# Performance work log

Measured on AMD Instinct MI355X. Metric: run time of the kernel, lower is better.

The kernel has to match this reference:

```python
import jax, jax.numpy as jnp
import numpy as np

B, T, D, H, DH, M, L, OUT = 512, 49, 256, 8, 32, 1024, 4, 151
DI = H * DH
THR = 0.02


def _ln(x, g, b):
    mu = x.mean(-1, keepdims=True)
    v = ((x - mu) ** 2).mean(-1, keepdims=True)
    return (x - mu) / jnp.sqrt(v + 1e-5) * g + b


def setup_inputs() -> dict:
    key = jax.random.key(0)
    ks = iter(jax.random.split(key, 64))

    def W(*s):
        return jax.random.normal(next(ks), s, jnp.float32) * 0.02

    inp = {}
    for n in ['img0', 'img1', 'p0', 'p1', 'p2']:
        inp[n] = jax.random.normal(next(ks), (B, T, D), jnp.float32)
    inp['idx'] = jax.random.randint(next(ks), (3, 2, B, T), 0, T, dtype=jnp.int32)
    # two transformer encoders (image/point), stacked over [encoder=2, layer=L]
    inp['enc_ln1g'] = jnp.ones((2, L, D)); inp['enc_ln1b'] = jnp.zeros((2, L, D))
    inp['enc_wqkv'] = W(2, L, D, 3 * DI)
    inp['enc_wo'] = W(2, L, DI, D); inp['enc_bo'] = jnp.zeros((2, L, D))
    inp['enc_ln2g'] = jnp.ones((2, L, D)); inp['enc_ln2b'] = jnp.zeros((2, L, D))
    inp['enc_w1'] = W(2, L, D, M); inp['enc_b1'] = jnp.zeros((2, L, M))
    inp['enc_w2'] = W(2, L, M, D); inp['enc_b2'] = jnp.zeros((2, L, D))
    # per-depth score nets (PredictorLG)
    inp['sc_lng'] = jnp.ones((L, D)); inp['sc_lnb'] = jnp.zeros((L, D))
    inp['sc_w1'] = W(L, D, D); inp['sc_b1'] = jnp.zeros((L, D))
    inp['sc_w2'] = W(L, D, D // 2); inp['sc_b2'] = jnp.zeros((L, D // 2))
    inp['sc_w3'] = W(L, D // 2, 2); inp['sc_b3'] = jnp.zeros((L, 2))
    # per-depth patch MLPs (FFN dim->mlp_dim->mlp_dim->dim, 3 layers)
    inp['pm_w1'] = W(L, D, M); inp['pm_b1'] = jnp.zeros((L, M))
    inp['pm_w2'] = W(L, M, M); inp['pm_b2'] = jnp.zeros((L, M))
    inp['pm_w3'] = W(L, M, D); inp['pm_b3'] = jnp.zeros((L, D))
    # mlp head
    inp['hd_lng'] = jnp.ones((D,)); inp['hd_lnb'] = jnp.zeros((D,))
    inp['hd_w1'] = W(D, M); inp['hd_b1'] = jnp.zeros((M,))
    inp['hd_w2'] = W(M, OUT); inp['hd_b2'] = jnp.zeros((OUT,))
    return inp


def reference(img0, img1, p0, p1, p2, idx,
              enc_ln1g, enc_ln1b, enc_wqkv, enc_wo, enc_bo,
              enc_ln2g, enc_ln2b, enc_w1, enc_b1, enc_w2, enc_b2,
              sc_lng, sc_lnb, sc_w1, sc_b1, sc_w2, sc_b2, sc_w3, sc_b3,
              pm_w1, pm_b1, pm_w2, pm_b2, pm_w3, pm_b3,
              hd_lng, hd_lnb, hd_w1, hd_b1, hd_w2, hd_b2):

    def layer(x, e, i):
        # pre-norm attention
        h = _ln(x, enc_ln1g[e, i], enc_ln1b[e, i])
        qkv = h @ enc_wqkv[e, i]                      # [B,T,3*DI]
        q, k, v = jnp.split(qkv, 3, axis=-1)
        q = q.reshape(B, T, H, DH); k = k.reshape(B, T, H, DH); v = v.reshape(B, T, H, DH)
        a = jax.nn.softmax(jnp.einsum('bqhd,bkhd->bhqk', q, k) * (DH ** -0.5), -1)
        o = jnp.einsum('bhqk,bkhd->bqhd', a, v).reshape(B, T, DI)
        x = x + o @ enc_wo[e, i] + enc_bo[e, i]
        # pre-norm FFN
        h = _ln(x, enc_ln2g[e, i], enc_ln2b[e, i])
        return x + jax.nn.gelu(h @ enc_w1[e, i] + enc_b1[e, i]) @ enc_w2[e, i] + enc_b2[e, i]

    image_feats = [img0, img1]
    point_feats = [p0, p1, p2]
    pred_scores = []
    for i in range(L):
        image_tokens = [layer(f, 0, i) for f in image_feats]
        point_tokens = [layer(f, 1, i) for f in point_feats]
        allt = jnp.concatenate(image_tokens + point_tokens, axis=1)  # [B, 5*T, D]
        h = _ln(allt, sc_lng[i], sc_lnb[i])
        h = jax.nn.gelu(h @ sc_w1[i] + sc_b1[i])
        h = jax.nn.gelu(h @ sc_w2[i] + sc_b2[i])
        scores = jax.nn.softmax(h @ sc_w3[i] + sc_b3[i], -1)[:, :, 0]  # [B, 5*T]
        pred_scores.append(scores)
        mask = (scores > THR).astype(jnp.int32)[..., None]            # [B,5*T,1]
        fm = mask.astype(allt.dtype)
        fnm = (-mask - 1).astype(allt.dtype)  # torch ~int_mask is bitwise NOT: ~1=-2, ~0=-1 (faithful)
        image_feats = [image_tokens[j] * fm[:, j * T:(j + 1) * T]
                       + image_tokens[1 - j] * fnm[:, j * T:(j + 1) * T] for j in range(2)]

        def patch_mlp(x):
            h2 = jax.nn.gelu(x @ pm_w1[i] + pm_b1[i])
            h2 = jax.nn.gelu(h2 @ pm_w2[i] + pm_b2[i])
            return h2 @ pm_w3[i] + pm_b3[i]

        new_p = []
        for k2 in range(3):
            s0 = 2 * T + k2 * T
            g0 = jnp.take_along_axis(image_tokens[0], idx[k2, 0][..., None], axis=1)
            g1 = jnp.take_along_axis(image_tokens[1], idx[k2, 1][..., None], axis=1)
            patch = patch_mlp(g0) + patch_mlp(g1)
            new_p.append(point_tokens[k2] * fm[:, s0:s0 + T] + patch * fnm[:, s0:s0 + T])
        point_feats = new_p

    pooled = jnp.concatenate(image_feats + point_feats, axis=1).max(axis=1)  # [B, D]
    h = _ln(pooled, hd_lng, hd_lnb)
    smplx = jax.nn.gelu(h @ hd_w1 + hd_b1) @ hd_w2 + hd_b2                   # [B, OUT]
    pred_score = jnp.concatenate(pred_scores, axis=1)                         # [B, L*5*T]
    return smplx, pred_score
```

## Files before the change

kernel.cpp:

```cpp
#include <hip/hip_runtime.h>
#include <math.h>

#define B_ 512
#define T_ 49
#define D_ 256
#define M_ 1024
#define L_ 4
#define OUT_ 151
#define BT_ 25088
#define NTOK5 (5*BT_)
#define THRESH 0.02f

typedef __bf16 bf16x8 __attribute__((ext_vector_type(8)));
typedef float f32x4 __attribute__((ext_vector_type(4)));
typedef unsigned short us;

__device__ __forceinline__ float gelu_t(float x){
    float u = 0.7978845608028654f * x * (1.0f + 0.044715f*x*x);
    float e = __expf(-2.0f*u);
    return __fdividef(x, 1.0f + e);
}
__device__ __forceinline__ us f2bf(float f){
    unsigned int u = __float_as_uint(f);
    u += 0x7fffu + ((u>>16)&1u);
    return (us)(u>>16);
}
__device__ __forceinline__ float bf2f(us h){
    return __uint_as_float(((unsigned int)h)<<16);
}
__device__ __forceinline__ void gload16(const void* g, void* l){
    __builtin_amdgcn_global_load_lds(
        (const __attribute__((address_space(1))) void*)g,
        (__attribute__((address_space(3))) void*)l, 16, 0, 0);
}

__global__ void copy_in_kernel(const float* __restrict__ a0, const float* __restrict__ a1,
                               const float* __restrict__ a2, const float* __restrict__ a3,
                               const float* __restrict__ a4, float* __restrict__ dst){
    size_t i = (size_t)blockIdx.x*256 + threadIdx.x;
    if (i >= (size_t)NTOK5*64) return;
    int slot = (int)(i / ((size_t)BT_*64));
    size_t off = i % ((size_t)BT_*64);
    const float* src = slot==0?a0: slot==1?a1: slot==2?a2: slot==3?a3: a4;
    ((float4*)dst)[i] = ((const float4*)src)[off];
}

__global__ void xcvt_kernel(const float* __restrict__ x, us* __restrict__ y, int nrows){
    size_t i = (size_t)blockIdx.x*256 + threadIdx.x;
    if (i >= (size_t)nrows*64) return;
    float4 v = ((const float4*)x)[i];
    ushort4 o; o.x=f2bf(v.x); o.y=f2bf(v.y); o.z=f2bf(v.z); o.w=f2bf(v.w);
    ((ushort4*)y)[i] = o;
}

template<bool OBF>
__global__ void ln_kernel(const float* __restrict__ x, const float* __restrict__ g,
                          const float* __restrict__ b, void* __restrict__ y, int nrows){
    int row = blockIdx.x*4 + (threadIdx.x>>6);
    if (row >= nrows) return;
    int lane = threadIdx.x & 63;
    float4 v = ((const float4*)(x + (size_t)row*D_))[lane];
    float s  = v.x+v.y+v.z+v.w;
    float sq = v.x*v.x + v.y*v.y + v.z*v.z + v.w*v.w;
    #pragma unroll
    for (int o=32;o;o>>=1){ s += __shfl_xor(s,o,64); sq += __shfl_xor(sq,o,64); }
    float mu = s*(1.0f/256.0f);
    float rstd = rsqrtf(sq*(1.0f/256.0f) - mu*mu + 1e-5f);
    float4 gv = ((const float4*)g)[lane];
    float4 bv = ((const float4*)b)[lane];
    float o0 = (v.x-mu)*rstd*gv.x + bv.x;
    float o1 = (v.y-mu)*rstd*gv.y + bv.y;
    float o2 = (v.z-mu)*rstd*gv.z + bv.z;
    float o3 = (v.w-mu)*rstd*gv.w + bv.w;
    if (OBF){
        ushort4 o4; o4.x=f2bf(o0); o4.y=f2bf(o1); o4.z=f2bf(o2); o4.w=f2bf(o3);
        ((ushort4*)((us*)y + (size_t)row*D_))[lane] = o4;
    } else {
        float4 o4; o4.x=o0; o4.y=o1; o4.z=o2; o4.w=o3;
        ((float4*)((float*)y + (size_t)row*D_))[lane] = o4;
    }
}

__global__ void wtrans_kernel(const float* __restrict__ W, us* __restrict__ Wt,
                              int K, int N){
    int g = blockIdx.z;
    __shared__ float t[32][33];
    int k0 = blockIdx.y*32, n0 = blockIdx.x*32;
    int tx = threadIdx.x&31, ty = threadIdx.x>>5;
    for (int r=ty; r<32; r+=8){
        int k = k0+r, n = n0+tx;
        t[r][tx] = (k<K && n<N) ? W[(size_t)g*K*N + (size_t)k*N + n] : 0.f;
    }
    __syncthreads();
    for (int r=ty; r<32; r+=8){
        int n = n0+r, k = k0+tx;
        if (n<N && k<K) Wt[(size_t)g*N*K + (size_t)n*K + k] = f2bf(t[tx][r]);
    }
}

__global__ void wtrans_pad_kernel(const float* __restrict__ W, us* __restrict__ Wt,
                                  int K, int Nsrc, int Ndst){
    __shared__ float t[32][33];
    int k0 = blockIdx.y*32, n0 = blockIdx.x*32;
    int tx = threadIdx.x&31, ty = threadIdx.x>>5;
    for (int r=ty; r<32; r+=8){
        int k = k0+r, n = n0+tx;
        t[r][tx] = (k<K && n<Nsrc) ? W[(size_t)k*Nsrc + n] : 0.f;
    }
    __syncthreads();
    for (int r=ty; r<32; r+=8){
        int n = n0+r, k = k0+tx;
        if (n<Ndst && k<K) Wt[(size_t)n*K + k] = f2bf(t[tx][r]);
    }
}

__global__ void padb_kernel(const float* __restrict__ b, float* __restrict__ o,
                            int Nsrc, int Ndst){
    int i = blockIdx.x*256 + threadIdx.x;
    if (i < Ndst) o[i] = (i < Nsrc) ? b[i] : 0.f;
}

__global__ void headcopy_kernel(const float* __restrict__ src, float* __restrict__ dst){
    int i = blockIdx.x*256 + threadIdx.x;
    if (i >= B_*OUT_) return;
    int r = i / OUT_, c = i % OUT_;
    dst[i] = src[(size_t)r*256 + c];
}

__device__ __forceinline__ void gemm_compute(const us* As, const us* Bs,
        int wr, int wc, int lr, int kg, f32x4 (&acc)[4][4]){
    bf16x8 av[4], bv[4];
    #pragma unroll
    for (int mi=0;mi<4;mi++){
        int r = wr*64 + mi*16 + lr;
        av[mi] = *(const bf16x8*)(&As[r*32 + ((kg ^ ((r>>1)&3))<<3)]);
    }
    #pragma unroll
    for (int ni=0;ni<4;ni++){
        int c = wc*64 + ni*16 + lr;
        bv[ni] = *(const bf16x8*)(&Bs[c*32 + ((kg ^ ((c>>1)&3))<<3)]);
    }
    #pragma unroll
    for (int mi=0;mi<4;mi++)
        #pragma unroll
        for (int ni=0;ni<4;ni++)
            acc[mi][ni] = __builtin_amdgcn_mfma_f32_16x16x32_bf16(av[mi], bv[ni], acc[mi][ni], 0, 0, 0);
}

template<int ACT, int RIN, bool OBF>
__global__ __launch_bounds__(256) void mfma_gemm(
    const us* __restrict__ A, const us* __restrict__ Wt,
    const float* __restrict__ bias, const void* __restrict__ resid,
    void* __restrict__ Cout, int Mr, int N, int K)
{
    __shared__ __align__(16) us SM[3*8192];
    const int nwg  = gridDim.x*gridDim.y;
    const int flat = blockIdx.y*gridDim.x + blockIdx.x;
    const int qq = nwg>>3, rr = nwg&7;
    const int xcd = flat&7, sidx = flat>>3;
    const int logical = (xcd<rr) ? (xcd*(qq+1)+sidx) : (rr*(qq+1)+(xcd-rr)*qq+sidx);
    const int bn = (logical % gridDim.x)*128;
    const int bm = (logical / gridDim.x)*128;
    const int tid = threadIdx.x;
    const int lane = tid&63, w = tid>>6;
    const int wr = w>>1, wc = w&1;
    const int lr = lane&15, kg = lane>>4;
    f32x4 acc[4][4] = {};

    const int j0 = tid, j1 = tid+256;
    const int row0 = j0>>2, row1 = j1>>2;
    const int k8s0 = (j0&3) ^ ((row0>>1)&3);
    const int k8s1 = (j1&3) ^ ((row1>>1)&3);
    int ga0 = bm+row0; if (ga0>=Mr) ga0=Mr-1;
    int ga1 = bm+row1; if (ga1>=Mr) ga1=Mr-1;
    int gb0 = bn+row0; if (gb0>=N) gb0=N-1;
    int gb1 = bn+row1; if (gb1>=N) gb1=N-1;
    const us* a0p = A  + (size_t)ga0*K + k8s0*8;
    const us* a1p = A  + (size_t)ga1*K + k8s1*8;
    const us* b0p = Wt + (size_t)gb0*K + k8s0*8;
    const us* b1p = Wt + (size_t)gb1*K + k8s1*8;

    const int nk = K >> 5;
    #define STAGEK(t_) { us* nb_ = SM + ((t_)%3)*8192; int k0_ = (t_)<<5; \
        gload16(a0p + k0_, nb_ + j0*8); \
        gload16(a1p + k0_, nb_ + j1*8); \
        gload16(b0p + k0_, nb_ + 4096 + j0*8); \
        gload16(b1p + k0_, nb_ + 4096 + j1*8); }
    STAGEK(0); STAGEK(1);
    for (int t=0; t<nk; ++t){
        if (t+1 < nk) asm volatile("s_waitcnt vmcnt(4)" ::: "memory");
        else          asm volatile("s_waitcnt vmcnt(0)" ::: "memory");
        __builtin_amdgcn_s_barrier();
        __builtin_amdgcn_sched_barrier(0);
        if (t+2 < nk) STAGEK(t+2);
        const us* cb = SM + (t%3)*8192;
        gemm_compute(cb, cb+4096, wr, wc, lr, kg, acc);
    }
    #undef STAGEK
    __syncthreads();

    if (OBF && RIN==0){
        us* Cs16 = (us*)SM;
        #pragma unroll
        for (int mi=0;mi<4;mi++){
            #pragma unroll
            for (int ni=0;ni<4;ni++){
                #pragma unroll
                for (int r4=0;r4<4;r4++){
                    int row = wr*64 + mi*16 + kg*4 + r4;
                    int col = wc*64 + ni*16 + lr;
                    float v = acc[mi][ni][r4];
                    if (bias) v += bias[bn + col];
                    if (ACT==1) v = gelu_t(v);
                    int h = ((row>>2)&3) | ((row&1)<<2);
                    int punit = (col>>3) ^ h;
                    Cs16[row*128 + punit*8 + (col&7)] = f2bf(v);
                }
            }
        }
        __syncthreads();
        {
            int rbase = tid>>3, seg = tid&7;
            #pragma unroll
            for (int pass=0; pass<8; ++pass){
                int row = rbase + (pass>>1)*32;
                int half = pass&1;
                int grow = bm + row;
                if (grow < Mr){
                    int h = ((row>>2)&3) | ((row&1)<<2);
                    int punit = (half*8+seg) ^ h;
                    *(uint4*)((us*)Cout + (size_t)grow*N + bn + half*64 + seg*8)
                        = *(const uint4*)&Cs16[row*128 + punit*8];
                }
            }
        }
        return;
    }

    float* Cs = (float*)SM;
    #pragma unroll
    for (int er=0; er<2; er++){
        #pragma unroll
        for (int ml=0; ml<2; ml++){
            int mi = er*2 + ml;
            #pragma unroll
            for (int ni=0;ni<4;ni++){
                #pragma unroll
                for (int r4=0;r4<4;r4++){
                    int lrow = wr*32 + ml*16 + kg*4 + r4;
                    int lcol = wc*64 + ni*16 + lr;
                    int pcol = lcol ^ (((lrow>>2)&1)<<4);
                    float v = acc[mi][ni][r4];
                    if (bias) v += bias[bn + lcol];
                    if (ACT==1) v = gelu_t(v);
                    Cs[lrow*128 + pcol] = v;
                }
            }
        }
        __syncthreads();
        #pragma unroll
        for (int s=0; s<2; s++){
            int lrow = (tid>>3) + s*32;
            int tseg = tid&7;
            int pseg = tseg ^ ((lrow>>2)&1);
            const float4* src = (const float4*)&Cs[lrow*128 + pseg*16];
            float4 v0=src[0], v1=src[1], v2=src[2], v3=src[3];
            int grow = bm + (lrow>>5)*64 + (er*2 + ((lrow>>4)&1))*16 + (lrow&15);
            int gcol = bn + tseg*16;
            if (grow < Mr){
                if (RIN==1){
                    const float4* rp = (const float4*)((const float*)resid + (size_t)grow*N + gcol);
                    float4 r0=rp[0], r1=rp[1], r2=rp[2], r3=rp[3];
                    v0.x+=r0.x; v0.y+=r0.y; v0.z+=r0.z; v0.w+=r0.w;
                    v1.x+=r1.x; v1.y+=r1.y; v1.z+=r1.z; v1.w+=r1.w;
                    v2.x+=r2.x; v2.y+=r2.y; v2.z+=r2.z; v2.w+=r2.w;
                    v3.x+=r3.x; v3.y+=r3.y; v3.z+=r3.z; v3.w+=r3.w;
                } else if (RIN==2){
                    const uint4* rp = (const uint4*)((const us*)resid + (size_t)grow*N + gcol);
                    uint4 u0=rp[0], u1=rp[1];
                    v0.x+=bf2f((us)(u0.x&0xffff)); v0.y+=bf2f((us)(u0.x>>16));
                    v0.z+=bf2f((us)(u0.y&0xffff)); v0.w+=bf2f((us)(u0.y>>16));
                    v1.x+=bf2f((us)(u0.z&0xffff)); v1.y+=bf2f((us)(u0.z>>16));
                    v1.z+=bf2f((us)(u0.w&0xffff)); v1.w+=bf2f((us)(u0.w>>16));
                    v2.x+=bf2f((us)(u1.x&0xffff)); v2.y+=bf2f((us)(u1.x>>16));
                    v2.z+=bf2f((us)(u1.y&0xffff)); v2.w+=bf2f((us)(u1.y>>16));
                    v3.x+=bf2f((us)(u1.z&0xffff)); v3.y+=bf2f((us)(u1.z>>16));
                    v3.z+=bf2f((us)(u1.w&0xffff)); v3.w+=bf2f((us)(u1.w>>16));
                }
                if (OBF){
                    unsigned int w0 = (unsigned)f2bf(v0.x) | ((unsigned)f2bf(v0.y)<<16);
                    unsigned int w1 = (unsigned)f2bf(v0.z) | ((unsigned)f2bf(v0.w)<<16);
                    unsigned int w2 = (unsigned)f2bf(v1.x) | ((unsigned)f2bf(v1.y)<<16);
                    unsigned int w3 = (unsigned)f2bf(v1.z) | ((unsigned)f2bf(v1.w)<<16);
                    unsigned int w4 = (unsigned)f2bf(v2.x) | ((unsigned)f2bf(v2.y)<<16);
                    unsigned int w5 = (unsigned)f2bf(v2.z) | ((unsigned)f2bf(v2.w)<<16);
                    unsigned int w6 = (unsigned)f2bf(v3.x) | ((unsigned)f2bf(v3.y)<<16);
                    unsigned int w7 = (unsigned)f2bf(v3.z) | ((unsigned)f2bf(v3.w)<<16);
                    uint4* op = (uint4*)((us*)Cout + (size_t)grow*N + gcol);
                    uint4 u0; u0.x=w0; u0.y=w1; u0.z=w2; u0.w=w3;
                    uint4 u1; u1.x=w4; u1.y=w5; u1.z=w6; u1.w=w7;
                    op[0]=u0; op[1]=u1;
                } else {
                    float4* op = (float4*)((float*)Cout + (size_t)grow*N + gcol);
                    op[0]=v0; op[1]=v1; op[2]=v2; op[3]=v3;
                }
            }
        }
        __syncthreads();
    }
}

__global__ __launch_bounds__(128) void attn_kernel(const us* __restrict__ qkv,
                                                   us* __restrict__ o){
    __shared__ float ks[2][T_][36], vs[2][T_][36];
    const int w = threadIdx.x >> 6, lane = threadIdx.x & 63;
    const int bh = blockIdx.x*2 + w;
    const int bb = bh >> 3, h = bh & 7;
    const us* base = qkv + (size_t)bb*T_*768 + h*32;
    if (lane < T_){
        const uint4* kp = (const uint4*)(base + (size_t)lane*768 + 256);
        const uint4* vp = (const uint4*)(base + (size_t)lane*768 + 512);
        #pragma unroll
        for (int j=0;j<4;j++){
            uint4 ku = kp[j], vu = vp[j];
            unsigned ka[4]={ku.x,ku.y,ku.z,ku.w}, va[4]={vu.x,vu.y,vu.z,vu.w};
            #pragma unroll
            for (int e=0;e<4;e++){
                ks[w][lane][j*8+e*2]   = bf2f((us)(ka[e]&0xffffu));
                ks[w][lane][j*8+e*2+1] = bf2f((us)(ka[e]>>16));
                vs[w][lane][j*8+e*2]   = bf2f((us)(va[e]&0xffffu));
                vs[w][lane][j*8+e*2+1] = bf2f((us)(va[e]>>16));
            }
        }
    }
    __syncthreads();
    if (lane >= T_) return;
    float q[32];
    {
        const uint4* qp = (const uint4*)(base + (size_t)lane*768);
        #pragma unroll
        for (int j=0;j<4;j++){
            uint4 qu = qp[j];
            unsigned qa[4]={qu.x,qu.y,qu.z,qu.w};
            #pragma unroll
            for (int e=0;e<4;e++){
                q[j*8+e*2]   = bf2f((us)(qa[e]&0xffffu));
                q[j*8+e*2+1] = bf2f((us)(qa[e]>>16));
            }
        }
    }
    float S[T_];
    #pragma unroll
    for (int c=0;c<T_;c++){
        float acc = 0.f;
        #pragma unroll
        for (int d=0;d<32;d++) acc += q[d]*ks[w][c][d];
        S[c] = acc*0.17677669529663687f;
    }
    float m = S[0];
    #pragma unroll
    for (int c=1;c<T_;c++) m = fmaxf(m, S[c]);
    float sum = 0.f;
    #pragma unroll
    for (int c=0;c<T_;c++){ S[c] = __expf(S[c]-m); sum += S[c]; }
    float inv = __fdividef(1.f, sum);
    float oa[32];
    #pragma unroll
    for (int d=0;d<32;d++) oa[d] = 0.f;
    #pragma unroll
    for (int c=0;c<T_;c++){
        float p2 = S[c]*inv;
        #pragma unroll
        for (int d=0;d<32;d++) oa[d] += p2*vs[w][c][d];
    }
    unsigned* op = (unsigned*)(o + ((size_t)bb*T_ + lane)*256 + h*32);
    #pragma unroll
    for (int j=0;j<16;j++)
        op[j] = (unsigned)f2bf(oa[2*j]) | ((unsigned)f2bf(oa[2*j+1])<<16);
}

__global__ void score_kernel(const us* __restrict__ s2, const float* __restrict__ w3,
                             const float* __restrict__ b3, float* __restrict__ sc,
                             float* __restrict__ pred, int layer, int row0, int nrows){
    int lr = blockIdx.x*256 + threadIdx.x;
    if (lr >= nrows) return;
    int row = row0 + lr;
    int s = row / BT_;
    int r = row % BT_;
    int b = r / T_;
    int t = r % T_;
    const uint4* xv = (const uint4*)(s2 + (size_t)lr*128);
    float l0 = b3[0], l1 = b3[1];
    #pragma unroll
    for (int q=0;q<16;q++){
        uint4 u = xv[q];
        unsigned int uu[4] = {u.x,u.y,u.z,u.w};
        #pragma unroll
        for (int e=0;e<4;e++){
            float fa = bf2f((us)(uu[e]&0xffff));
            float fb = bf2f((us)(uu[e]>>16));
            int d = q*8 + e*2;
            l0 += fa*w3[d*2]     + fb*w3[(d+1)*2];
            l1 += fa*w3[d*2+1]   + fb*w3[(d+1)*2+1];
        }
    }
    float m = fmaxf(l0,l1);
    float e0 = __expf(l0-m), e1 = __expf(l1-m);
    float sc0 = __fdividef(e0, e0+e1);
    sc[b*(5*T_) + s*T_ + t] = sc0;
    pred[(size_t)b*(L_*5*T_) + (size_t)layer*(5*T_) + s*T_ + t] = sc0;
}

__global__ void img_fuse_kernel(float* __restrict__ X, const float* __restrict__ sc){
    size_t i = (size_t)blockIdx.x*256 + threadIdx.x;
    if (i >= (size_t)BT_*64) return;
    int row = (int)(i>>6), d4 = (int)(i&63);
    int b = row / T_, t = row % T_;
    float s0 = sc[b*(5*T_) + t];
    float s1 = sc[b*(5*T_) + T_ + t];
    float fm0  = (s0 > THRESH)? 1.f : 0.f;
    float fnm0 = -fm0 - 1.f;
    float fm1  = (s1 > THRESH)? 1.f : 0.f;
    float fnm1 = -fm1 - 1.f;
    float4* p0 = ((float4*)(X + (size_t)row*D_)) + d4;
    float4* p1 = ((float4*)(X + ((size_t)BT_ + row)*D_)) + d4;
    float4 a0 = *p0, a1 = *p1;
    float4 r0, r1;
    r0.x = a0.x*fm0 + a1.x*fnm0;  r0.y = a0.y*fm0 + a1.y*fnm0;
    r0.z = a0.z*fm0 + a1.z*fnm0;  r0.w = a0.w*fm0 + a1.w*fnm0;
    r1.x = a1.x*fm1 + a0.x*fnm1;  r1.y = a1.y*fm1 + a0.y*fnm1;
    r1.z = a1.z*fm1 + a0.z*fnm1;  r1.w = a1.w*fm1 + a0.w*fnm1;
    *p0 = r0; *p1 = r1;
}

__global__ void pt_fuse_gather_kernel(float* __restrict__ X, const us* __restrict__ PM,
                                      const int* __restrict__ idx, const float* __restrict__ sc){
    size_t i = (size_t)blockIdx.x*256 + threadIdx.x;
    if (i >= (size_t)3*BT_*64) return;
    int vrow = (int)(i>>6), d4 = (int)(i&63);
    int k2 = vrow / BT_, grow = vrow % BT_;
    int b = grow / T_, t = grow % T_;
    float s = sc[b*(5*T_) + (2+k2)*T_ + t];
    float fm  = (s > THRESH)? 1.f : 0.f;
    float fnm = -fm - 1.f;
    int i0 = idx[(size_t)(k2*2+0)*BT_ + grow];
    int i1 = idx[(size_t)(k2*2+1)*BT_ + grow];
    uint2 u0 = ((const uint2*)(PM + ((size_t)b*T_ + i0)*D_))[d4];
    uint2 u1 = ((const uint2*)(PM + ((size_t)BT_ + (size_t)b*T_ + i1)*D_))[d4];
    float p0 = bf2f((us)(u0.x&0xffff)) + bf2f((us)(u1.x&0xffff));
    float p1 = bf2f((us)(u0.x>>16))    + bf2f((us)(u1.x>>16));
    float p2 = bf2f((us)(u0.y&0xffff)) + bf2f((us)(u1.y&0xffff));
    float p3 = bf2f((us)(u0.y>>16))    + bf2f((us)(u1.y>>16));
    float4* xp = ((float4*)(X + ((size_t)(2+k2)*BT_ + grow)*D_)) + d4;
    float4 a = *xp;
    float4 rr;
    rr.x = a.x*fm + p0*fnm;
    rr.y = a.y*fm + p1*fnm;
    rr.z = a.z*fm + p2*fnm;
    rr.w = a.w*fm + p3*fnm;
    *xp = rr;
}

__global__ void pool_kernel(const float* __restrict__ x, float* __restrict__ p){
    int i = blockIdx.x*256 + threadIdx.x;
    if (i >= B_*64) return;
    int b = i>>6, d4 = i&63;
    float4 m; m.x=m.y=m.z=m.w=-3.4e38f;
    for (int s=0;s<5;s++){
        const float4* bp = ((const float4*)(x + ((size_t)s*BT_ + (size_t)b*T_)*D_)) + d4;
        for (int t=0;t<T_;t++){
            float4 v = bp[(size_t)t*64];
            m.x=fmaxf(m.x,v.x); m.y=fmaxf(m.y,v.y); m.z=fmaxf(m.z,v.z); m.w=fmaxf(m.w,v.w);
        }
    }
    ((float4*)p)[i] = m;
}

static inline int cdiv(int a, int b){ return (a+b-1)/b; }

extern "C" void kernel_launch(void* const* d_in, const int* in_sizes, int n_in,
                              void* d_out, int out_size, void* d_ws, size_t ws_size,
                              hipStream_t stream)
{
    const float* in_img0 = (const float*)d_in[0];
    const float* in_img1 = (const float*)d_in[1];
    const float* in_p0   = (const float*)d_in[2];
    const float* in_p1   = (const float*)d_in[3];
    const float* in_p2   = (const float*)d_in[4];
    const int*   in_idx  = (const int*)d_in[5];
    const float* enc_ln1g = (const float*)d_in[6];
    const float* enc_ln1b = (const float*)d_in[7];
    const float* enc_wqkv = (const float*)d_in[8];
    const float* enc_wo   = (const float*)d_in[9];
    const float* enc_bo   = (const float*)d_in[10];
    const float* enc_ln2g = (const float*)d_in[11];
    const float* enc_ln2b = (const float*)d_in[12];
    const float* enc_w1   = (const float*)d_in[13];
    const float* enc_b1   = (const float*)d_in[14];
    const float* enc_w2   = (const float*)d_in[15];
    const float* enc_b2   = (const float*)d_in[16];
    const float* sc_lng   = (const float*)d_in[17];
    const float* sc_lnb   = (const float*)d_in[18];
    const float* sc_w1    = (const float*)d_in[19];
    const float* sc_b1    = (const float*)d_in[20];
    const float* sc_w2    = (const float*)d_in[21];
    const float* sc_b2    = (const float*)d_in[22];
    const float* sc_w3    = (const float*)d_in[23];
    const float* sc_b3    = (const float*)d_in[24];
    const float* pm_w1    = (const float*)d_in[25];
    const float* pm_b1    = (const float*)d_in[26];
    const float* pm_w2    = (const float*)d_in[27];
    const float* pm_b2    = (const float*)d_in[28];
    const float* pm_w3    = (const float*)d_in[29];
    const float* pm_b3    = (const float*)d_in[30];
    const float* hd_lng   = (const float*)d_in[31];
    const float* hd_lnb   = (const float*)d_in[32];
    const float* hd_w1    = (const float*)d_in[33];
    const float* hd_b1    = (const float*)d_in[34];
    const float* hd_w2    = (const float*)d_in[35];
    const float* hd_b2    = (const float*)d_in[36];

    char* p = (char*)d_ws;
    float* X   = (float*)p;  p += (size_t)5*BT_*D_*4;
    float* SCb = (float*)p;  p += (size_t)B_*5*T_*4;
    us* PM   = (us*)p; p += (size_t)2*BT_*D_*2;
    us* WQKV = (us*)p; p += (size_t)8*768*256*2;
    us* WWO  = (us*)p; p += (size_t)8*256*256*2;
    us* WW1  = (us*)p; p += (size_t)8*1024*256*2;
    us* WW2  = (us*)p; p += (size_t)8*256*1024*2;
    us* WS1  = (us*)p; p += (size_t)4*256*256*2;
    us* WS2  = (us*)p; p += (size_t)4*128*256*2;
    us* WP1  = (us*)p; p += (size_t)4*1024*256*2;
    us* WP2  = (us*)p; p += (size_t)4*1024*1024*2;
    us* WP3  = (us*)p; p += (size_t)4*256*1024*2;
    us* WH1  = (us*)p; p += (size_t)1024*256*2;
    us* WH2  = (us*)p; p += (size_t)256*1024*2;
    float* B2P  = (float*)p; p += (size_t)256*4;
    float* POOL = (float*)p; p += (size_t)B_*256*4;
    us*    HLNb = (us*)p;  p += (size_t)B_*256*2;
    us*    HMIDb= (us*)p;  p += (size_t)B_*1024*2;
    float* HOUT = (float*)p; p += (size_t)B_*256*4;
    size_t fixed = (size_t)(p - (char*)d_ws);
    long long poolb = (long long)ws_size - (long long)fixed;
    if (poolb < 0) poolb = 0;
    auto chunkOf = [&](long long perRow, int maxRows)->int{
        long long c = poolb / perRow;
        c = (c / T_) * T_;
        if (c < T_) c = T_;
        if (c > maxRows) c = maxRows;
        return (int)c;
    };
    auto evenC = [&](int total, int Cmax)->int{
        int nch = (total + Cmax - 1)/Cmax;
        int per = (total + nch - 1)/nch;
        per = ((per + T_ - 1)/T_)*T_;
        if (per > Cmax) per = Cmax;
        return per;
    };
    int CencMax = chunkOf(2560, 3*BT_);
    int CscMax  = chunkOf(1024, NTOK5);
    int CpmMax  = chunkOf(4096, 2*BT_);
    char* pb = p;
    us* eR1 = (us*)pb;
    us* eR2 = (us*)(pb + (size_t)CencMax*512);
    us* eR3 = eR1;
    us* sR1 = (us*)pb;
    us* sS1 = (us*)(pb + (size_t)CscMax*512);
    us* sS2 = sR1;
    us* m1  = (us*)pb;
    us* m2  = (us*)(pb + (size_t)CpmMax*2048);
    us* cA  = m2;

    float* out_smplx = (float*)d_out;
    float* out_pred  = out_smplx + (size_t)B_*OUT_;

    wtrans_kernel<<<dim3(cdiv(768,32), cdiv(256,32), 8),256,0,stream>>>(enc_wqkv, WQKV, 256, 768);
    wtrans_kernel<<<dim3(cdiv(256,32), cdiv(256,32), 8),256,0,stream>>>(enc_wo,   WWO,  256, 256);
    wtrans_kernel<<<dim3(cdiv(1024,32),cdiv(256,32), 8),256,0,stream>>>(enc_w1,   WW1,  256, 1024);
    wtrans_kernel<<<dim3(cdiv(256,32), cdiv(1024,32),8),256,0,stream>>>(enc_w2,   WW2,  1024,256);
    wtrans_kernel<<<dim3(cdiv(256,32), cdiv(256,32), 4),256,0,stream>>>(sc_w1,    WS1,  256, 256);
    wtrans_kernel<<<dim3(cdiv(128,32), cdiv(256,32), 4),256,0,stream>>>(sc_w2,    WS2,  256, 128);
    wtrans_kernel<<<dim3(cdiv(1024,32),cdiv(256,32), 4),256,0,stream>>>(pm_w1,    WP1,  256, 1024);
    wtrans_kernel<<<dim3(cdiv(1024,32),cdiv(1024,32),4),256,0,stream>>>(pm_w2,    WP2,  1024,1024);
    wtrans_kernel<<<dim3(cdiv(256,32), cdiv(1024,32),4),256,0,stream>>>(pm_w3,    WP3,  1024,256);
    wtrans_kernel<<<dim3(cdiv(1024,32),cdiv(256,32), 1),256,0,stream>>>(hd_w1,    WH1,  256, 1024);
    wtrans_pad_kernel<<<dim3(cdiv(256,32), cdiv(1024,32)),256,0,stream>>>(hd_w2, WH2, 1024, 151, 256);
    padb_kernel<<<1,256,0,stream>>>(hd_b2, B2P, 151, 256);

    copy_in_kernel<<<cdiv(NTOK5*64,256), 256, 0, stream>>>(in_img0,in_img1,in_p0,in_p1,in_p2, X);

    for (int i=0;i<L_;i++){
        for (int grp=0; grp<2; grp++){
            int base  = (grp==0)? 0 : 2*BT_;
            int total = (grp==0)? 2*BT_ : 3*BT_;
            size_t wi = (size_t)(grp*L_ + i);
            int C = evenC(total, CencMax);
            for (int off=0; off<total; off+=C){
                int R = total-off < C ? total-off : C;
                float* Xp = X + (size_t)(base+off)*D_;
                ln_kernel<true><<<cdiv(R,4),256,0,stream>>>(Xp, enc_ln1g+wi*D_, enc_ln1b+wi*D_, eR1, R);
                mfma_gemm<0,0,true><<<dim3(6, cdiv(R,128)),256,0,stream>>>(
                    eR1, WQKV + wi*768*256, nullptr, nullptr, eR2, R, 768, 256);
                attn_kernel<<<(R/T_)*4,128,0,stream>>>(eR2, eR3);
                mfma_gemm<0,1,false><<<dim3(2, cdiv(R,128)),256,0,stream>>>(
                    eR3, WWO + wi*256*256, enc_bo + wi*D_, Xp, Xp, R, 256, 256);
                ln_kernel<true><<<cdiv(R,4),256,0,stream>>>(Xp, enc_ln2g+wi*D_, enc_ln2b+wi*D_, eR1, R);
                mfma_gemm<1,0,true><<<dim3(8, cdiv(R,128)),256,0,stream>>>(
                    eR1, WW1 + wi*1024*256, enc_b1 + wi*M_, nullptr, eR2, R, 1024, 256);
                mfma_gemm<0,1,false><<<dim3(2, cdiv(R,128)),256,0,stream>>>(
                    eR2, WW2 + wi*256*1024, enc_b2 + wi*D_, Xp, Xp, R, 256, 1024);
            }
        }
        {
            int C = evenC(NTOK5, CscMax);
            for (int off=0; off<NTOK5; off+=C){
                int R = NTOK5-off < C ? NTOK5-off : C;
                ln_kernel<true><<<cdiv(R,4),256,0,stream>>>(X + (size_t)off*D_,
                    sc_lng+(size_t)i*D_, sc_lnb+(size_t)i*D_, sR1, R);
                mfma_gemm<1,0,true><<<dim3(2, cdiv(R,128)),256,0,stream>>>(
                    sR1, WS1 + (size_t)i*256*256, sc_b1+(size_t)i*D_, nullptr, sS1, R, 256, 256);
                mfma_gemm<1,0,true><<<dim3(1, cdiv(R,128)),256,0,stream>>>(
                    sS1, WS2 + (size_t)i*128*256, sc_b2+(size_t)i*128, nullptr, sS2, R, 128, 256);
                score_kernel<<<cdiv(R,256),256,0,stream>>>(
                    sS2, sc_w3+(size_t)i*256, sc_b3+(size_t)i*2, SCb, out_pred, i, off, R);
            }
        }
        {
            int C = evenC(2*BT_, CpmMax);
            for (int off=0; off<2*BT_; off+=C){
                int R = 2*BT_-off < C ? 2*BT_-off : C;
                xcvt_kernel<<<cdiv(R*64,256),256,0,stream>>>(X + (size_t)off*D_, cA, R);
                mfma_gemm<1,0,true><<<dim3(8, cdiv(R,128)),256,0,stream>>>(
                    cA, WP1 + (size_t)i*1024*256, pm_b1+(size_t)i*M_, nullptr, m1, R, 1024, 256);
                mfma_gemm<1,0,true><<<dim3(8, cdiv(R,128)),256,0,stream>>>(
                    m1, WP2 + (size_t)i*1024*1024, pm_b2+(size_t)i*M_, nullptr, m2, R, 1024, 1024);
                mfma_gemm<0,0,true><<<dim3(2, cdiv(R,128)),256,0,stream>>>(
                    m2, WP3 + (size_t)i*256*1024, pm_b3+(size_t)i*D_, nullptr, PM + (size_t)off*D_, R, 256, 1024);
            }
        }
        pt_fuse_gather_kernel<<<cdiv(3*BT_*64,256),256,0,stream>>>(X, PM, in_idx, SCb);
        img_fuse_kernel<<<cdiv(BT_*64,256),256,0,stream>>>(X, SCb);
    }
    pool_kernel<<<cdiv(B_*64,256),256,0,stream>>>(X, POOL);
    ln_kernel<true><<<cdiv(B_,4),256,0,stream>>>(POOL, hd_lng, hd_lnb, HLNb, B_);
    mfma_gemm<1,0,true><<<dim3(8, cdiv(B_,128)),256,0,stream>>>(
        HLNb, WH1, hd_b1, nullptr, HMIDb, B_, 1024, 256);
    mfma_gemm<0,0,false><<<dim3(2, cdiv(B_,128)),256,0,stream>>>(
        HMIDb, WH2, B2P, nullptr, HOUT, B_, 256, 1024);
    headcopy_kernel<<<cdiv(B_*OUT_,256),256,0,stream>>>(HOUT, out_smplx);
}
```

Baseline: 6.092 ms.

## Add wide 128x256-tile MFMA GEMM with XCD-aware block remap for bf16-output GEMMs

Adds a new GEMM kernel with 128x256 output tiles, a triple-buffered LDS pipeline with swizzled loads, an XCD-aware remapping of workgroup indices, and a staged, swizzled shared-memory epilogue that writes coalesced bf16 rows. All bf16-output GEMMs (QKV, FFN1, score layer 1, patch MLP, head layer 1) switch to it with half as many column blocks. The aim is more operand reuse per loaded tile, better L2 locality across XCDs, and wider stores. The cost is larger per-block register and LDS use (4x8 accumulators per wave, about 72KB LDS), which may lower occupancy.

```diff
diff --git a/kernel.cpp b/kernel.cpp
--- a/kernel.cpp
+++ b/kernel.cpp
@@ -307,6 +307,107 @@
             }
         }
         __syncthreads();
+    }
+}
+
+template<int ACT>
+__global__ __launch_bounds__(256,2) void mfma_gemm_w(
+    const us* __restrict__ A, const us* __restrict__ Wt,
+    const float* __restrict__ bias, us* __restrict__ Cout,
+    int Mr, int N, int K)
+{
+    __shared__ __align__(16) us SM[3*12288];
+    const int nwg  = gridDim.x*gridDim.y;
+    const int flat = blockIdx.y*gridDim.x + blockIdx.x;
+    const int qq = nwg>>3, rr = nwg&7;
+    const int xcd = flat&7, sidx = flat>>3;
+    const int logical = (xcd<rr) ? (xcd*(qq+1)+sidx) : (rr*(qq+1)+(xcd-rr)*qq+sidx);
+    const int bn = (logical % gridDim.x)*256;
+    const int bm = (logical / gridDim.x)*128;
+    const int tid = threadIdx.x;
+    const int lane = tid&63, w = tid>>6;
+    const int wr = w>>1, wc = w&1;
+    const int lr = lane&15, kg = lane>>4;
+    f32x4 acc[4][8] = {};
+
+    const us *aA0, *aA1, *aB0, *aB1, *aB2, *aB3;
+    { int j=tid;     int row=j>>2, s8=(j&3)^((row>>1)&3); int g=bm+row; if(g>=Mr)g=Mr-1; aA0 = A  + (size_t)g*K + s8*8; }
+    { int j=tid+256; int row=j>>2, s8=(j&3)^((row>>1)&3); int g=bm+row; if(g>=Mr)g=Mr-1; aA1 = A  + (size_t)g*K + s8*8; }
+    { int j=tid;     int row=j>>2, s8=(j&3)^((row>>1)&3); int g=bn+row; if(g>=N) g=N-1;  aB0 = Wt + (size_t)g*K + s8*8; }
+    { int j=tid+256; int row=j>>2, s8=(j&3)^((row>>1)&3); int g=bn+row; if(g>=N) g=N-1;  aB1 = Wt + (size_t)g*K + s8*8; }
+    { int j=tid+512; int row=j>>2, s8=(j&3)^((row>>1)&3); int g=bn+row; if(g>=N) g=N-1;  aB2 = Wt + (size_t)g*K + s8*8; }
+    { int j=tid+768; int row=j>>2, s8=(j&3)^((row>>1)&3); int g=bn+row; if(g>=N) g=N-1;  aB3 = Wt + (size_t)g*K + s8*8; }
+
+    const int nk = K >> 5;
+    #define STAGEW(t_) { us* nb_ = SM + ((t_)%3)*12288; int k0_ = (t_)<<5; \
+        gload16(aA0 + k0_, nb_ + (size_t)tid*8); \
+        gload16(aA1 + k0_, nb_ + (size_t)(tid+256)*8); \
+        gload16(aB0 + k0_, nb_ + 4096 + (size_t)tid*8); \
+        gload16(aB1 + k0_, nb_ + 4096 + (size_t)(tid+256)*8); \
+        gload16(aB2 + k0_, nb_ + 4096 + (size_t)(tid+512)*8); \
+        gload16(aB3 + k0_, nb_ + 4096 + (size_t)(tid+768)*8); }
+    STAGEW(0); STAGEW(1);
+    for (int t=0; t<nk; ++t){
+        if (t+1 < nk) asm volatile("s_waitcnt vmcnt(6)" ::: "memory");
+        else          asm volatile("s_waitcnt vmcnt(0)" ::: "memory");
+        __builtin_amdgcn_s_barrier();
+        __builtin_amdgcn_sched_barrier(0);
+        if (t+2 < nk) STAGEW(t+2);
+        const us* cb = SM + (t%3)*12288;
+        const us* Bb = cb + 4096;
+        bf16x8 av[4], bv[8];
+        #pragma unroll
+        for (int mi=0;mi<4;mi++){
+            int r = wr*64 + mi*16 + lr;
+            av[mi] = *(const bf16x8*)(&cb[r*32 + ((kg ^ ((r>>1)&3))<<3)]);
+        }
+        #pragma unroll
+        for (int ni=0;ni<8;ni++){
+            int c = wc*128 + ni*16 + lr;
+            bv[ni] = *(const bf16x8*)(&Bb[c*32 + ((kg ^ ((c>>1)&3))<<3)]);
+        }
+        #pragma unroll
+        for (int mi=0;mi<4;mi++)
+            #pragma unroll
+            for (int ni=0;ni<8;ni++)
+                acc[mi][ni] = __builtin_amdgcn_mfma_f32_16x16x32_bf16(av[mi], bv[ni], acc[mi][ni], 0, 0, 0);
+    }
+    #undef STAGEW
+    __syncthreads();
+
+    us* Cs16 = (us*)SM;
+    #pragma unroll
+    for (int mi=0;mi<4;mi++){
+        #pragma unroll
+        for (int ni=0;ni<8;ni++){
+            #pragma unroll
+            for (int r4=0;r4<4;r4++){
+                int row = wr*64 + mi*16 + kg*4 + r4;
+                int col = wc*128 + ni*16 + lr;
+                float v = acc[mi][ni][r4];
+                if (bias) v += bias[bn + col];
+                if (ACT==1) v = gelu_t(v);
+                int h = ((row>>2)&3) | ((row&1)<<2);
+                int punit = (col>>3) ^ h;
+                Cs16[row*256 + punit*8 + (col&7)] = f2bf(v);
+            }
+        }
+    }
+    __syncthreads();
+    {
+        int rbase = tid>>3, seg = tid&7;
+        #pragma unroll
+        for (int pass=0; pass<16; ++pass){
+            int row = rbase + (pass&3)*32;
+            int useg = (pass>>2)*8 + seg;
+            int grow = bm + row;
+            if (grow < Mr){
+                int h = ((row>>2)&3) | ((row&1)<<2);
+                int punit = useg ^ h;
+                *(uint4*)(Cout + (size_t)grow*N + bn + useg*8)
+                    = *(const uint4*)&Cs16[row*256 + punit*8];
+            }
+        }
     }
 }
 
@@ -599,14 +700,14 @@
                 int R = total-off < C ? total-off : C;
                 float* Xp = X + (size_t)(base+off)*D_;
                 ln_kernel<true><<<cdiv(R,4),256,0,stream>>>(Xp, enc_ln1g+wi*D_, enc_ln1b+wi*D_, eR1, R);
-                mfma_gemm<0,0,true><<<dim3(6, cdiv(R,128)),256,0,stream>>>(
-                    eR1, WQKV + wi*768*256, nullptr, nullptr, eR2, R, 768, 256);
+                mfma_gemm_w<0><<<dim3(3, cdiv(R,128)),256,0,stream>>>(
+                    eR1, WQKV + wi*768*256, nullptr, eR2, R, 768, 256);
                 attn_kernel<<<(R/T_)*4,128,0,stream>>>(eR2, eR3);
                 mfma_gemm<0,1,false><<<dim3(2, cdiv(R,128)),256,0,stream>>>(
                     eR3, WWO + wi*256*256, enc_bo + wi*D_, Xp, Xp, R, 256, 256);
                 ln_kernel<true><<<cdiv(R,4),256,0,stream>>>(Xp, enc_ln2g+wi*D_, enc_ln2b+wi*D_, eR1, R);
-                mfma_gemm<1,0,true><<<dim3(8, cdiv(R,128)),256,0,stream>>>(
-                    eR1, WW1 + wi*1024*256, enc_b1 + wi*M_, nullptr, eR2, R, 1024, 256);
+                mfma_gemm_w<1><<<dim3(4, cdiv(R,128)),256,0,stream>>>(
+                    eR1, WW1 + wi*1024*256, enc_b1 + wi*M_, eR2, R, 1024, 256);
                 mfma_gemm<0,1,false><<<dim3(2, cdiv(R,128)),256,0,stream>>>(
                     eR2, WW2 + wi*256*1024, enc_b2 + wi*D_, Xp, Xp, R, 256, 1024);
             }
@@ -617,8 +718,8 @@
                 int R = NTOK5-off < C ? NTOK5-off : C;
                 ln_kernel<true><<<cdiv(R,4),256,0,stream>>>(X + (size_t)off*D_,
                     sc_lng+(size_t)i*D_, sc_lnb+(size_t)i*D_, sR1, R);
-                mfma_gemm<1,0,true><<<dim3(2, cdiv(R,128)),256,0,stream>>>(
-                    sR1, WS1 + (size_t)i*256*256, sc_b1+(size_t)i*D_, nullptr, sS1, R, 256, 256);
+                mfma_gemm_w<1><<<dim3(1, cdiv(R,128)),256,0,stream>>>(
+                    sR1, WS1 + (size_t)i*256*256, sc_b1+(size_t)i*D_, sS1, R, 256, 256);
                 mfma_gemm<1,0,true><<<dim3(1, cdiv(R,128)),256,0,stream>>>(
                     sS1, WS2 + (size_t)i*128*256, sc_b2+(size_t)i*128, nullptr, sS2, R, 128, 256);
                 score_kernel<<<cdiv(R,256),256,0,stream>>>(
@@ -630,12 +731,12 @@
             for (int off=0; off<2*BT_; off+=C){
                 int R = 2*BT_-off < C ? 2*BT_-off : C;
                 xcvt_kernel<<<cdiv(R*64,256),256,0,stream>>>(X + (size_t)off*D_, cA, R);
-                mfma_gemm<1,0,true><<<dim3(8, cdiv(R,128)),256,0,stream>>>(
-                    cA, WP1 + (size_t)i*1024*256, pm_b1+(size_t)i*M_, nullptr, m1, R, 1024, 256);
-                mfma_gemm<1,0,true><<<dim3(8, cdiv(R,128)),256,0,stream>>>(
-                    m1, WP2 + (size_t)i*1024*1024, pm_b2+(size_t)i*M_, nullptr, m2, R, 1024, 1024);
-                mfma_gemm<0,0,true><<<dim3(2, cdiv(R,128)),256,0,stream>>>(
-                    m2, WP3 + (size_t)i*256*1024, pm_b3+(size_t)i*D_, nullptr, PM + (size_t)off*D_, R, 256, 1024);
+                mfma_gemm_w<1><<<dim3(4, cdiv(R,128)),256,0,stream>>>(
+                    cA, WP1 + (size_t)i*1024*256, pm_b1+(size_t)i*M_, m1, R, 1024, 256);
+                mfma_gemm_w<1><<<dim3(4, cdiv(R,128)),256,0,stream>>>(
+                    m1, WP2 + (size_t)i*1024*1024, pm_b2+(size_t)i*M_, m2, R, 1024, 1024);
+                mfma_gemm_w<0><<<dim3(1, cdiv(R,128)),256,0,stream>>>(
+                    m2, WP3 + (size_t)i*256*1024, pm_b3+(size_t)i*D_, PM + (size_t)off*D_, R, 256, 1024);
             }
         }
         pt_fuse_gather_kernel<<<cdiv(3*BT_*64,256),256,0,stream>>>(X, PM, in_idx, SCb);
@@ -643,8 +744,8 @@
     }
     pool_kernel<<<cdiv(B_*64,256),256,0,stream>>>(X, POOL);
     ln_kernel<true><<<cdiv(B_,4),256,0,stream>>>(POOL, hd_lng, hd_lnb, HLNb, B_);
-    mfma_gemm<1,0,true><<<dim3(8, cdiv(B_,128)),256,0,stream>>>(
-        HLNb, WH1, hd_b1, nullptr, HMIDb, B_, 1024, 256);
+    mfma_gemm_w<1><<<dim3(4, cdiv(B_,128)),256,0,stream>>>(
+        HLNb, WH1, hd_b1, HMIDb, B_, 1024, 256);
     mfma_gemm<0,0,false><<<dim3(2, cdiv(B_,128)),256,0,stream>>>(
         HMIDb, WH2, B2P, nullptr, HOUT, B_, 256, 1024);
     headcopy_kernel<<<cdiv(B_*OUT_,256),256,0,stream>>>(HOUT, out_smplx);
```

After: 6.952 ms. 1.14x slower.
